# Optimization experiments

Hardware: AMD Instinct MI355X
Metric: run time of the kernel (lower is better)

The kernel has to match this reference:

```python
import jax, jax.numpy as jnp
import numpy as np
import math

B, L, D, H, FF = 32, 512, 512, 8, 2048
DH = D // H
EPS = 1e-5

def pe_table(L, D):
    pos = jnp.arange(L, dtype=jnp.float32)[:, None]
    div = jnp.exp(jnp.arange(0, D, 2, dtype=jnp.float32) * (-(math.log(10000.0) / D)))
    pe = jnp.zeros((L, D), dtype=jnp.float32)
    pe = pe.at[:, 0::2].set(jnp.sin(pos * div))
    pe = pe.at[:, 1::2].set(jnp.cos(pos * div))
    return pe

def setup_inputs() -> dict:
    key = jax.random.key(0)
    ks = jax.random.split(key, 16)
    s = 0.02
    inp = {
        "x": jax.random.normal(ks[0], (B, L, D), jnp.float32),
        "mask": jnp.ones((B, L), jnp.int32),
        "speaker_emb": jax.random.normal(ks[1], (B, L, D), jnp.float32),
        "Wg": jax.random.normal(ks[2], (D, D), jnp.float32) * s,
        "Wq": jax.random.normal(ks[3], (D, D), jnp.float32) * s,
        "bq": jnp.zeros((D,), jnp.float32),
        "Wk": jax.random.normal(ks[4], (D, D), jnp.float32) * s,
        "bk": jnp.zeros((D,), jnp.float32),
        "Wv": jax.random.normal(ks[5], (D, D), jnp.float32) * s,
        "bv": jnp.zeros((D,), jnp.float32),
        "Wo": jax.random.normal(ks[6], (D, D), jnp.float32) * s,
        "bo": jnp.zeros((D,), jnp.float32),
        "ln_g": jnp.ones((D,), jnp.float32),
        "ln_b": jnp.zeros((D,), jnp.float32),
        "W1": jax.random.normal(ks[7], (FF, D), jnp.float32) * s,
        "b1": jnp.zeros((FF,), jnp.float32),
        "W2": jax.random.normal(ks[8], (D, FF), jnp.float32) * s,
        "b2": jnp.zeros((D,), jnp.float32),
    }
    return inp

def layer_norm(x, g, b):
    mu = jnp.mean(x, axis=-1, keepdims=True)
    var = jnp.var(x, axis=-1, keepdims=True)
    return (x - mu) * jax.lax.rsqrt(var + EPS) * g + b

def reference(x, mask, speaker_emb, Wg, Wq, bq, Wk, bk, Wv, bv, Wo, bo, ln_g, ln_b, W1, b1, W2, b2):
    # DynamicGating: sigmoid(x W^T) * x
    x = jax.nn.sigmoid(x @ Wg.T) * x
    # speaker embedding + sinusoidal positional encoding (dropout is eval/no-op)
    x = x + speaker_emb + pe_table(L, D)[None, :, :]
    # Multi-head self-attention (eager, full score matrix)
    q = (x @ Wq.T + bq).reshape(B, L, H, DH).transpose(0, 2, 1, 3) / math.sqrt(DH)
    k = (x @ Wk.T + bk).reshape(B, L, H, DH).transpose(0, 2, 1, 3)
    v = (x @ Wv.T + bv).reshape(B, L, H, DH).transpose(0, 2, 1, 3)
    scores = jnp.einsum("bhqd,bhkd->bhqk", q, k)  # (B,H,L,L)
    key_mask = (mask == 0)[:, None, None, :]  # mask keys where mask==0
    scores = jnp.where(key_mask, jnp.float32(-1e10), scores)
    attn = jax.nn.softmax(scores, axis=-1)
    ctx = jnp.einsum("bhqk,bhkd->bhqd", attn, v)
    ctx = ctx.transpose(0, 2, 1, 3).reshape(B, L, D)
    attn_out = ctx @ Wo.T + bo
    h = attn_out + x  # residual (dropout no-op)
    # FeedForwardNet: note GELU applied after BOTH linears (faithful to source)
    mid = jax.nn.gelu(layer_norm(h, ln_g, ln_b) @ W1.T + b1, approximate=True)
    out = jax.nn.gelu(mid @ W2.T + b2, approximate=True)
    return out + h
```

## Files before the change

### kernel.cpp

```cpp
#include <hip/hip_runtime.h>
#include <math.h>

#define Bn 32
#define Ln 512
#define Dn 512
#define Hn 8
#define DHn 64
#define FFn 2048
#define Mn (Bn*Ln)
#define QKVS 1536

typedef __attribute__((ext_vector_type(4))) float f32x4;
typedef __attribute__((ext_vector_type(8))) short short8;

__device__ __forceinline__ float bf2f(ushort u){ return __uint_as_float(((unsigned)u) << 16); }
__device__ __forceinline__ ushort f2bf(float f){
  unsigned u = __float_as_uint(f);
  u += 0x7FFFu + ((u >> 16) & 1u);
  return (ushort)(u >> 16);
}
__device__ __forceinline__ float gelu_fast(float x){
  float y2 = 1.5957691216057308f * (x + 0.044715f*x*x*x);
  return x / (1.0f + __expf(-y2));
}

__device__ __forceinline__ void gload_lds16(const ushort* g, ushort* l){
  __builtin_amdgcn_global_load_lds(
      (__attribute__((address_space(1))) void*)(void*)g,
      (__attribute__((address_space(3))) void*)(void*)l, 16, 0, 0);
}

__device__ __forceinline__ void cvt4(const float* __restrict__ in, ushort* __restrict__ out, int u){
  float4 v = *(const float4*)(in + u*4);
  ushort4 o;
  o.x = f2bf(v.x); o.y = f2bf(v.y); o.z = f2bf(v.z); o.w = f2bf(v.w);
  *(ushort4*)(out + u*4) = o;
}

__global__ __launch_bounds__(256) void prep_kernel(
    const float* __restrict__ Wg, const float* __restrict__ Wq, const float* __restrict__ Wk,
    const float* __restrict__ Wv, const float* __restrict__ Wo, const float* __restrict__ W1,
    const float* __restrict__ W2,
    const float* __restrict__ bq, const float* __restrict__ bk, const float* __restrict__ bv,
    ushort* __restrict__ wgb, ushort* __restrict__ wqkvb, ushort* __restrict__ wob,
    ushort* __restrict__ w1b, ushort* __restrict__ w2b,
    float* __restrict__ pe, float* __restrict__ bqkv)
{
  int u = blockIdx.x*256 + threadIdx.x;
  const int WU = 65536, FU = 262144;
  if (u < WU){ cvt4(Wg, wgb, u); return; }            u -= WU;
  if (u < WU){ cvt4(Wq, wqkvb, u); return; }          u -= WU;
  if (u < WU){ cvt4(Wk, wqkvb + 262144, u); return; } u -= WU;
  if (u < WU){ cvt4(Wv, wqkvb + 524288, u); return; } u -= WU;
  if (u < WU){ cvt4(Wo, wob, u); return; }            u -= WU;
  if (u < FU){ cvt4(W1, w1b, u); return; }            u -= FU;
  if (u < FU){ cvt4(W2, w2b, u); return; }            u -= FU;
  if (u < WU){
    int e = u*4; int l = e >> 9; int d0 = e & 511;
    #pragma unroll
    for (int p=0;p<2;p++){
      int i = (d0 >> 1) + p;
      float dv = expf((float)(2*i) * (-9.210340371976184f/512.0f));
      float ang = (float)l * dv;
      pe[e + 2*p]     = sinf(ang);
      pe[e + 2*p + 1] = cosf(ang);
    }
    return;
  }
  u -= WU;
  if (u < 384){
    int e = u*4;
    #pragma unroll
    for (int j=0;j<4;j++){
      int i = e + j;
      bqkv[i] = (i < 512) ? bq[i] : (i < 1024) ? bk[i-512] : bv[i-1024];
    }
  }
}

__global__ void cvt_kernel(const float* __restrict__ in, ushort* __restrict__ out, int n){
  int i = (blockIdx.x*256 + threadIdx.x)*4;
  if (i >= n) return;
  cvt4(in, out, i >> 2);
}

template<int MODE>
__global__ __launch_bounds__(512) void gemm_kernel(
    const ushort* __restrict__ A, const ushort* __restrict__ W,
    const float* __restrict__ bias,
    const float* __restrict__ res,
    const ushort* __restrict__ rbf,
    const float* __restrict__ spk, const float* __restrict__ pe,
    float* __restrict__ outf, ushort* __restrict__ outb, ushort* __restrict__ outb2,
    int K, int N, int gx)
{
  __shared__ ushort lbuf[2][2][16384];
  int t = threadIdx.x;
  int wave = t >> 6, lane = t & 63;
  int wrow = wave >> 2, wcol = wave & 3;
  int g = lane >> 4, r16 = lane & 15;

  int nwg = gx * (Mn/256);
  int wg = blockIdx.x;
  int tile = (wg & 7)*(nwg >> 3) + (wg >> 3);
  int trow = tile / gx;
  int tcol = tile - trow*gx;
  int rowBase = trow * 256;
  int colBase = tcol * 256;

  int srow8 = lane >> 3;
  int sucol = ((lane & 7) ^ srow8) * 8;
  const ushort* gA = A + (size_t)(rowBase + wave*8 + srow8)*K + sucol;
  const ushort* gW = W + (size_t)(colBase + wave*8 + srow8)*K + sucol;

  f32x4 acc[8][4];
  #pragma unroll
  for (int m=0;m<8;m++)
    #pragma unroll
    for (int n=0;n<4;n++) acc[m][n] = (f32x4)0.0f;

  #pragma unroll
  for (int c=0;c<4;c++){
    gload_lds16(gA + (size_t)c*64*K, &lbuf[0][0][c*4096 + wave*512]);
    gload_lds16(gW + (size_t)c*64*K, &lbuf[0][1][c*4096 + wave*512]);
  }

  int cb = 0;
  for (int k0 = 0; k0 < K; k0 += 64){
    if (k0 + 64 < K){
      #pragma unroll
      for (int c=0;c<4;c++){
        gload_lds16(gA + (size_t)c*64*K + k0 + 64, &lbuf[cb^1][0][c*4096 + wave*512]);
        gload_lds16(gW + (size_t)c*64*K + k0 + 64, &lbuf[cb^1][1][c*4096 + wave*512]);
      }
      asm volatile("s_waitcnt vmcnt(8)" ::: "memory");
    } else {
      asm volatile("s_waitcnt vmcnt(0)" ::: "memory");
    }
    __builtin_amdgcn_s_barrier();
    #pragma unroll
    for (int ks=0; ks<2; ks++){
      short8 af[8], bfr[4];
      #pragma unroll
      for (int m=0;m<8;m++){
        int row = wrow*128 + m*16 + r16;
        af[m] = *(const short8*)&lbuf[cb][0][row*64 + (((ks<<2)+g) ^ (r16 & 7))*8];
      }
      #pragma unroll
      for (int n=0;n<4;n++){
        int row = wcol*64 + n*16 + r16;
        bfr[n] = *(const short8*)&lbuf[cb][1][row*64 + (((ks<<2)+g) ^ (r16 & 7))*8];
      }
      #pragma unroll
      for (int m=0;m<8;m++)
        #pragma unroll
        for (int n=0;n<4;n++)
          acc[m][n] = __builtin_amdgcn_mfma_f32_16x16x32_bf16(af[m], bfr[n], acc[m][n], 0, 0, 0);
    }
    __builtin_amdgcn_s_barrier();
    cb ^= 1;
  }

  if constexpr (MODE == 0 || MODE == 1 || MODE == 3){
    bool vpart = false;
    if constexpr (MODE == 1) vpart = (colBase >= 1024);
    if (!vpart){
      ushort* ct = &lbuf[0][0][0];
      #pragma unroll
      for (int m=0;m<8;m++){
        #pragma unroll
        for (int n=0;n<4;n++){
          int col = wcol*64 + n*16 + r16;
          int gc = colBase + col;
          float sc = 1.0f;
          if constexpr (MODE == 1) sc = (gc < 512) ? 0.125f : 1.0f;
          #pragma unroll
          for (int j=0;j<4;j++){
            int row = wrow*128 + m*16 + g*4 + j;
            float c = acc[m][n][j];
            ushort val;
            if constexpr (MODE == 0){
              int gr = rowBase + row;
              size_t o = (size_t)gr * N + gc;
              float s = 1.0f/(1.0f + __expf(-c));
              val = f2bf(s * res[o] + spk[o] + pe[(gr & (Ln-1))*Dn + gc]);
            } else if constexpr (MODE == 3){
              val = f2bf(gelu_fast(c + bias[gc]));
            } else {
              val = f2bf((c + bias[gc]) * sc);
            }
            ct[row*256 + (col ^ ((row & 7) << 3))] = val;
          }
        }
      }
      __syncthreads();
      int r = t >> 1, ch = (t & 1)*128;
      ushort* dst = outb + (size_t)(rowBase + r)*N + colBase + ch;
      #pragma unroll
      for (int q=0;q<16;q++){
        int col = (ch + q*8) ^ ((r & 7) << 3);
        *(short8*)(dst + q*8) = *(const short8*)&ct[r*256 + col];
      }
    } else {
      #pragma unroll
      for (int m=0;m<8;m++){
        #pragma unroll
        for (int n=0;n<4;n++){
          int gc = colBase + wcol*64 + n*16 + r16;
          int dhg = gc - 1024;
          int gr0 = rowBase + wrow*128 + m*16 + g*4;
          int bb = gr0 >> 9, l0 = gr0 & 511;
          ushort4 o4;
          o4.x = f2bf(acc[m][n][0] + bias[gc]);
          o4.y = f2bf(acc[m][n][1] + bias[gc]);
          o4.z = f2bf(acc[m][n][2] + bias[gc]);
          o4.w = f2bf(acc[m][n][3] + bias[gc]);
          *(ushort4*)(outb2 + ((size_t)(bb*Hn + (dhg>>6))*DHn + (dhg & 63))*Ln + l0) = o4;
        }
      }
    }
  } else {
    #pragma unroll
    for (int m=0;m<8;m++){
      #pragma unroll
      for (int n=0;n<4;n++){
        int gc = colBase + wcol*64 + n*16 + r16;
        #pragma unroll
        for (int j=0;j<4;j++){
          int gr = rowBase + wrow*128 + m*16 + g*4 + j;
          size_t o = (size_t)gr * N + gc;
          float c = acc[m][n][j];
          if constexpr (MODE == 2){
            outf[o] = c + bias[gc] + bf2f(rbf[o]);
          } else {
            outf[o] = gelu_fast(c + bias[gc]) + res[o];
          }
        }
      }
    }
  }
}

__global__ __launch_bounds__(256) void attn_mfma_kernel(
    const ushort* __restrict__ qb, const ushort* __restrict__ kb, const ushort* __restrict__ vtb,
    const int* __restrict__ mask, ushort* __restrict__ ctxb)
{
  __shared__ ushort lK[2][64][72];
  __shared__ ushort lVt[2][64][72];
  __shared__ ushort lP[4][32][72];

  int t = threadIdx.x;
  int w = t >> 6, lane = t & 63;
  int g = lane >> 4, r16 = lane & 15;
  int b = blockIdx.z, h = blockIdx.y;
  int qbase = blockIdx.x*128 + w*32;

  int key0 = t >> 3;
  int c8s = (t & 7) * 8;
  const ushort* kbase = kb + (size_t)(b*Ln)*QKVS + h*DHn + c8s;
  const ushort* vt = vtb + (size_t)((b*Hn + h)*DHn) * Ln;

  short8 af_q[2][2];
  #pragma unroll
  for (int m=0;m<2;m++)
    #pragma unroll
    for (int ks=0;ks<2;ks++)
      af_q[m][ks] = *(const short8*)(qb + (size_t)(b*Ln + qbase + m*16 + r16)*QKVS + h*DHn + ks*32 + g*8);

  f32x4 acc_ctx[2][4];
  #pragma unroll
  for (int m=0;m<2;m++)
    #pragma unroll
    for (int n=0;n<4;n++) acc_ctx[m][n] = (f32x4)0.0f;
  float mrun[2][4], lrun[2][4];
  #pragma unroll
  for (int m=0;m<2;m++)
    #pragma unroll
    for (int j=0;j<4;j++){ mrun[m][j] = -INFINITY; lrun[m][j] = 0.0f; }

  {
    short8 ka = *(const short8*)(kbase + (size_t)key0*QKVS);
    short8 kc = *(const short8*)(kbase + (size_t)(key0+32)*QKVS);
    short8 va = *(const short8*)(vt + (size_t)key0*Ln + c8s);
    short8 vc = *(const short8*)(vt + (size_t)(key0+32)*Ln + c8s);
    *(short8*)&lK[0][key0][c8s] = ka;
    *(short8*)&lK[0][key0+32][c8s] = kc;
    *(short8*)&lVt[0][key0][c8s] = va;
    *(short8*)&lVt[0][key0+32][c8s] = vc;
  }
  __syncthreads();
  int cb = 0;

  for (int kb0 = 0; kb0 < Ln; kb0 += 64){
    short8 kna, knb, vna, vnb;
    bool more = (kb0 + 64 < Ln);
    if (more){
      kna = *(const short8*)(kbase + (size_t)(kb0 + 64 + key0)*QKVS);
      knb = *(const short8*)(kbase + (size_t)(kb0 + 64 + key0 + 32)*QKVS);
      vna = *(const short8*)(vt + (size_t)key0*Ln + kb0 + 64 + c8s);
      vnb = *(const short8*)(vt + (size_t)(key0+32)*Ln + kb0 + 64 + c8s);
    }

    f32x4 acc_s[2][4];
    #pragma unroll
    for (int m=0;m<2;m++)
      #pragma unroll
      for (int n=0;n<4;n++) acc_s[m][n] = (f32x4)0.0f;
    __builtin_amdgcn_s_setprio(1);
    #pragma unroll
    for (int ks=0;ks<2;ks++){
      short8 bf_k[4];
      #pragma unroll
      for (int n=0;n<4;n++)
        bf_k[n] = *(const short8*)&lK[cb][n*16 + r16][ks*32 + g*8];
      #pragma unroll
      for (int m=0;m<2;m++)
        #pragma unroll
        for (int n=0;n<4;n++)
          acc_s[m][n] = __builtin_amdgcn_mfma_f32_16x16x32_bf16(af_q[m][ks], bf_k[n], acc_s[m][n], 0, 0, 0);
    }
    __builtin_amdgcn_s_setprio(0);

    #pragma unroll
    for (int n=0;n<4;n++){
      if (mask[b*Ln + kb0 + n*16 + r16] == 0){
        #pragma unroll
        for (int m=0;m<2;m++)
          #pragma unroll
          for (int j=0;j<4;j++) acc_s[m][n][j] = -1e10f;
      }
    }

    #pragma unroll
    for (int m=0;m<2;m++){
      #pragma unroll
      for (int j=0;j<4;j++){
        float tmax = fmaxf(fmaxf(acc_s[m][0][j], acc_s[m][1][j]),
                           fmaxf(acc_s[m][2][j], acc_s[m][3][j]));
        #pragma unroll
        for (int off=1; off<16; off<<=1) tmax = fmaxf(tmax, __shfl_xor(tmax, off));
        float newm = fmaxf(mrun[m][j], tmax);
        float alpha = __expf(mrun[m][j] - newm);
        float p0 = __expf(acc_s[m][0][j] - newm);
        float p1 = __expf(acc_s[m][1][j] - newm);
        float p2 = __expf(acc_s[m][2][j] - newm);
        float p3 = __expf(acc_s[m][3][j] - newm);
        float tsum = (p0+p1)+(p2+p3);
        #pragma unroll
        for (int off=1; off<16; off<<=1) tsum += __shfl_xor(tsum, off);
        lrun[m][j] = lrun[m][j]*alpha + tsum;
        mrun[m][j] = newm;
        #pragma unroll
        for (int n2=0;n2<4;n2++) acc_ctx[m][n2][j] *= alpha;
        int prow = m*16 + g*4 + j;
        lP[w][prow][0*16 + r16] = f2bf(p0);
        lP[w][prow][1*16 + r16] = f2bf(p1);
        lP[w][prow][2*16 + r16] = f2bf(p2);
        lP[w][prow][3*16 + r16] = f2bf(p3);
      }
    }

    __builtin_amdgcn_s_setprio(1);
    #pragma unroll
    for (int ks2=0;ks2<2;ks2++){
      short8 af_p[2], bf_v[4];
      #pragma unroll
      for (int m=0;m<2;m++)
        af_p[m] = *(const short8*)&lP[w][m*16 + r16][ks2*32 + g*8];
      #pragma unroll
      for (int n=0;n<4;n++)
        bf_v[n] = *(const short8*)&lVt[cb][n*16 + r16][ks2*32 + g*8];
      #pragma unroll
      for (int m=0;m<2;m++)
        #pragma unroll
        for (int n=0;n<4;n++)
          acc_ctx[m][n] = __builtin_amdgcn_mfma_f32_16x16x32_bf16(af_p[m], bf_v[n], acc_ctx[m][n], 0, 0, 0);
    }
    __builtin_amdgcn_s_setprio(0);

    if (more){
      *(short8*)&lK[cb^1][key0][c8s] = kna;
      *(short8*)&lK[cb^1][key0+32][c8s] = knb;
      *(short8*)&lVt[cb^1][key0][c8s] = vna;
      *(short8*)&lVt[cb^1][key0+32][c8s] = vnb;
    }
    __syncthreads();
    cb ^= 1;
  }

  #pragma unroll
  for (int m=0;m<2;m++){
    #pragma unroll
    for (int j=0;j<4;j++){
      float inv = 1.0f / lrun[m][j];
      int gr = qbase + m*16 + g*4 + j;
      #pragma unroll
      for (int n=0;n<4;n++){
        ctxb[(size_t)(b*Ln + gr)*Dn + h*DHn + n*16 + r16] = f2bf(acc_ctx[m][n][j] * inv);
      }
    }
  }
}

__global__ __launch_bounds__(256) void ln_kernel(
    const float* __restrict__ hbuf, const float* __restrict__ gamma, const float* __restrict__ beta,
    ushort* __restrict__ out)
{
  int row = blockIdx.x*4 + (threadIdx.x >> 6);
  int lane = threadIdx.x & 63;
  const float* p = hbuf + (size_t)row*Dn + lane*8;
  float4 a = *(const float4*)p;
  float4 c = *(const float4*)(p + 4);
  float v[8] = {a.x,a.y,a.z,a.w,c.x,c.y,c.z,c.w};
  float s = 0.f, ss = 0.f;
  #pragma unroll
  for (int j=0;j<8;j++){ s += v[j]; ss += v[j]*v[j]; }
  #pragma unroll
  for (int off=32; off>0; off>>=1){ s += __shfl_xor(s, off); ss += __shfl_xor(ss, off); }
  float mu = s * (1.0f/Dn);
  float var = ss * (1.0f/Dn) - mu*mu;
  float rstd = rsqrtf(var + 1e-5f);
  ushort o8[8];
  #pragma unroll
  for (int j=0;j<8;j++) o8[j] = f2bf((v[j]-mu)*rstd*gamma[lane*8+j] + beta[lane*8+j]);
  ushort* op = out + (size_t)row*Dn + lane*8;
  *(ushort4*)op       = make_ushort4(o8[0],o8[1],o8[2],o8[3]);
  *(ushort4*)(op + 4) = make_ushort4(o8[4],o8[5],o8[6],o8[7]);
}

extern "C" void kernel_launch(void* const* d_in, const int* in_sizes, int n_in,
                              void* d_out, int out_size, void* d_ws, size_t ws_size,
                              hipStream_t stream) {
  (void)in_sizes; (void)n_in; (void)out_size; (void)ws_size;
  const float* x    = (const float*)d_in[0];
  const int*   mask = (const int*)d_in[1];
  const float* spk  = (const float*)d_in[2];
  const float* Wg   = (const float*)d_in[3];
  const float* Wq   = (const float*)d_in[4];  const float* bq = (const float*)d_in[5];
  const float* Wk   = (const float*)d_in[6];  const float* bk = (const float*)d_in[7];
  const float* Wv   = (const float*)d_in[8];  const float* bv = (const float*)d_in[9];
  const float* Wo   = (const float*)d_in[10]; const float* bo = (const float*)d_in[11];
  const float* lng  = (const float*)d_in[12]; const float* lnbeta = (const float*)d_in[13];
  const float* W1   = (const float*)d_in[14]; const float* b1 = (const float*)d_in[15];
  const float* W2   = (const float*)d_in[16]; const float* b2 = (const float*)d_in[17];
  float* out = (float*)d_out;

  char* w = (char*)d_ws;
  size_t o = 0;
  ushort* xbf   = (ushort*)(w + o); o += (size_t)Mn*Dn*2;
  ushort* xinb  = (ushort*)(w + o); o += (size_t)Mn*Dn*2;
  ushort* qkvb  = (ushort*)(w + o); o += (size_t)Mn*QKVS*2;
  ushort* vtb   = (ushort*)(w + o); o += (size_t)Mn*Dn*2;
  ushort* ctxb  = (ushort*)(w + o); o += (size_t)Mn*Dn*2;
  float*  hbuf  = (float*)(w + o);  o += (size_t)Mn*Dn*4;
  ushort* lnbuf = (ushort*)(w + o); o += (size_t)Mn*Dn*2;
  ushort* wgb   = (ushort*)(w + o); o += (size_t)Dn*Dn*2;
  ushort* wqkvb = (ushort*)(w + o); o += (size_t)QKVS*Dn*2;
  ushort* wob   = (ushort*)(w + o); o += (size_t)Dn*Dn*2;
  ushort* w1b   = (ushort*)(w + o); o += (size_t)FFn*Dn*2;
  ushort* w2b   = (ushort*)(w + o); o += (size_t)Dn*FFn*2;
  float*  pebuf = (float*)(w + o);  o += (size_t)Ln*Dn*4;
  float*  bqkv  = (float*)(w + o);  o += (size_t)QKVS*4;
  ushort* midb  = xbf;

  hipLaunchKernelGGL(prep_kernel, dim3(3586), dim3(256), 0, stream,
                     Wg, Wq, Wk, Wv, Wo, W1, W2, bq, bk, bv,
                     wgb, wqkvb, wob, w1b, w2b, pebuf, bqkv);
  hipLaunchKernelGGL(cvt_kernel, dim3((Mn*Dn/4)/256), dim3(256), 0, stream, x, xbf, Mn*Dn);

  hipLaunchKernelGGL((gemm_kernel<0>), dim3((Dn/256)*(Mn/256)), dim3(512), 0, stream,
                     xbf, wgb, (const float*)nullptr, x, (const ushort*)nullptr, spk, pebuf,
                     (float*)nullptr, xinb, (ushort*)nullptr, Dn, Dn, Dn/256);
  hipLaunchKernelGGL((gemm_kernel<1>), dim3((QKVS/256)*(Mn/256)), dim3(512), 0, stream,
                     xinb, wqkvb, bqkv, (const float*)nullptr, (const ushort*)nullptr,
                     (const float*)nullptr, (const float*)nullptr,
                     (float*)nullptr, qkvb, vtb, Dn, QKVS, QKVS/256);
  hipLaunchKernelGGL(attn_mfma_kernel, dim3(Ln/128, Hn, Bn), dim3(256), 0, stream,
                     qkvb, qkvb + 512, vtb, mask, ctxb);
  hipLaunchKernelGGL((gemm_kernel<2>), dim3((Dn/256)*(Mn/256)), dim3(512), 0, stream,
                     ctxb, wob, bo, (const float*)nullptr, xinb, (const float*)nullptr,
                     (const float*)nullptr, hbuf, (ushort*)nullptr, (ushort*)nullptr, Dn, Dn, Dn/256);
  hipLaunchKernelGGL(ln_kernel, dim3(Mn/4), dim3(256), 0, stream, hbuf, lng, lnbeta, lnbuf);
  hipLaunchKernelGGL((gemm_kernel<3>), dim3((FFn/256)*(Mn/256)), dim3(512), 0, stream,
                     lnbuf, w1b, b1, (const float*)nullptr, (const ushort*)nullptr,
                     (const float*)nullptr, (const float*)nullptr,
                     (float*)nullptr, midb, (ushort*)nullptr, Dn, FFn, FFn/256);
  hipLaunchKernelGGL((gemm_kernel<4>), dim3((Dn/256)*(Mn/256)), dim3(512), 0, stream,
                     midb, w2b, b2, hbuf, (const ushort*)nullptr,
                     (const float*)nullptr, (const float*)nullptr,
                     out, (ushort*)nullptr, (ushort*)nullptr, FFn, Dn, Dn/256);
}
```

Baseline: 347.3 us.

## Use 256x128 GEMM tiles with three-stage LDS pipeline and MFMA priority

Narrows the GEMM output tile from 256x256 to 256x128, doubling the workgroup count. It replaces the double-buffered LDS loop with a three-stage ring so loads for tile k+2 are in flight while tile k is computed, and drops one barrier per iteration. It also raises wave priority around the MFMA block. The intent is better occupancy and CU fill on the small-N GEMMs and more latency hiding, at the cost of lower arithmetic intensity per tile and more redundant A-tile loads.

```diff
diff --git a/kernel.cpp b/kernel.cpp
--- a/kernel.cpp
+++ b/kernel.cpp
@@ -94,7 +94,7 @@
     float* __restrict__ outf, ushort* __restrict__ outb, ushort* __restrict__ outb2,
     int K, int N, int gx)
 {
-  __shared__ ushort lbuf[2][2][16384];
+  __shared__ ushort lbuf[3][24576];
   int t = threadIdx.x;
   int wave = t >> 6, lane = t & 63;
   int wrow = wave >> 2, wcol = wave & 3;
@@ -106,71 +106,84 @@
   int trow = tile / gx;
   int tcol = tile - trow*gx;
   int rowBase = trow * 256;
-  int colBase = tcol * 256;
+  int colBase = tcol * 128;
 
   int srow8 = lane >> 3;
   int sucol = ((lane & 7) ^ srow8) * 8;
   const ushort* gA = A + (size_t)(rowBase + wave*8 + srow8)*K + sucol;
   const ushort* gW = W + (size_t)(colBase + wave*8 + srow8)*K + sucol;
 
-  f32x4 acc[8][4];
+  int NT = K >> 6;
+
+  f32x4 acc[8][2];
   #pragma unroll
   for (int m=0;m<8;m++)
     #pragma unroll
-    for (int n=0;n<4;n++) acc[m][n] = (f32x4)0.0f;
-
-  #pragma unroll
-  for (int c=0;c<4;c++){
-    gload_lds16(gA + (size_t)c*64*K, &lbuf[0][0][c*4096 + wave*512]);
-    gload_lds16(gW + (size_t)c*64*K, &lbuf[0][1][c*4096 + wave*512]);
-  }
-
-  int cb = 0;
-  for (int k0 = 0; k0 < K; k0 += 64){
-    if (k0 + 64 < K){
-      #pragma unroll
-      for (int c=0;c<4;c++){
-        gload_lds16(gA + (size_t)c*64*K + k0 + 64, &lbuf[cb^1][0][c*4096 + wave*512]);
-        gload_lds16(gW + (size_t)c*64*K + k0 + 64, &lbuf[cb^1][1][c*4096 + wave*512]);
-      }
-      asm volatile("s_waitcnt vmcnt(8)" ::: "memory");
-    } else {
-      asm volatile("s_waitcnt vmcnt(0)" ::: "memory");
-    }
-    __builtin_amdgcn_s_barrier();
+    for (int n=0;n<2;n++) acc[m][n] = (f32x4)0.0f;
+
+  #pragma unroll
+  for (int c=0;c<4;c++) gload_lds16(gA + (size_t)c*64*K,      &lbuf[0][c*4096 + wave*512]);
+  #pragma unroll
+  for (int c=0;c<2;c++) gload_lds16(gW + (size_t)c*64*K,      &lbuf[0][16384 + c*4096 + wave*512]);
+  #pragma unroll
+  for (int c=0;c<4;c++) gload_lds16(gA + (size_t)c*64*K + 64, &lbuf[1][c*4096 + wave*512]);
+  #pragma unroll
+  for (int c=0;c<2;c++) gload_lds16(gW + (size_t)c*64*K + 64, &lbuf[1][16384 + c*4096 + wave*512]);
+  asm volatile("s_waitcnt vmcnt(6)" ::: "memory");
+  __builtin_amdgcn_s_barrier();
+
+  int cur = 0, stg = 2;
+  for (int kt = 0; kt < NT; ++kt){
+    if (kt + 2 < NT){
+      int k0 = (kt + 2) << 6;
+      #pragma unroll
+      for (int c=0;c<4;c++) gload_lds16(gA + (size_t)c*64*K + k0, &lbuf[stg][c*4096 + wave*512]);
+      #pragma unroll
+      for (int c=0;c<2;c++) gload_lds16(gW + (size_t)c*64*K + k0, &lbuf[stg][16384 + c*4096 + wave*512]);
+    }
+    const ushort* ab = &lbuf[cur][0];
+    const ushort* bb = &lbuf[cur][16384];
+    __builtin_amdgcn_s_setprio(1);
     #pragma unroll
     for (int ks=0; ks<2; ks++){
-      short8 af[8], bfr[4];
+      short8 af[8], bfr[2];
       #pragma unroll
       for (int m=0;m<8;m++){
         int row = wrow*128 + m*16 + r16;
-        af[m] = *(const short8*)&lbuf[cb][0][row*64 + (((ks<<2)+g) ^ (r16 & 7))*8];
-      }
-      #pragma unroll
-      for (int n=0;n<4;n++){
-        int row = wcol*64 + n*16 + r16;
-        bfr[n] = *(const short8*)&lbuf[cb][1][row*64 + (((ks<<2)+g) ^ (r16 & 7))*8];
+        af[m] = *(const short8*)&ab[row*64 + (((ks<<2)+g) ^ (row & 7))*8];
+      }
+      #pragma unroll
+      for (int n=0;n<2;n++){
+        int row = wcol*32 + n*16 + r16;
+        bfr[n] = *(const short8*)&bb[row*64 + (((ks<<2)+g) ^ (row & 7))*8];
       }
       #pragma unroll
       for (int m=0;m<8;m++)
         #pragma unroll
-        for (int n=0;n<4;n++)
+        for (int n=0;n<2;n++)
           acc[m][n] = __builtin_amdgcn_mfma_f32_16x16x32_bf16(af[m], bfr[n], acc[m][n], 0, 0, 0);
     }
-    __builtin_amdgcn_s_barrier();
-    cb ^= 1;
+    __builtin_amdgcn_s_setprio(0);
+    if (kt + 1 < NT){
+      if (kt + 2 < NT) asm volatile("s_waitcnt vmcnt(6)" ::: "memory");
+      else             asm volatile("s_waitcnt vmcnt(0)" ::: "memory");
+      __builtin_amdgcn_s_barrier();
+    }
+    cur = (cur == 2) ? 0 : cur + 1;
+    stg = (stg == 2) ? 0 : stg + 1;
   }
 
   if constexpr (MODE == 0 || MODE == 1 || MODE == 3){
     bool vpart = false;
     if constexpr (MODE == 1) vpart = (colBase >= 1024);
     if (!vpart){
-      ushort* ct = &lbuf[0][0][0];
+      __syncthreads();
+      ushort* ct = &lbuf[0][0];
       #pragma unroll
       for (int m=0;m<8;m++){
         #pragma unroll
-        for (int n=0;n<4;n++){
-          int col = wcol*64 + n*16 + r16;
+        for (int n=0;n<2;n++){
+          int col = wcol*32 + n*16 + r16;
           int gc = colBase + col;
           float sc = 1.0f;
           if constexpr (MODE == 1) sc = (gc < 512) ? 0.125f : 1.0f;
@@ -189,33 +202,33 @@
             } else {
               val = f2bf((c + bias[gc]) * sc);
             }
-            ct[row*256 + (col ^ ((row & 7) << 3))] = val;
+            ct[row*128 + (col ^ ((row & 7) << 3))] = val;
           }
         }
       }
       __syncthreads();
-      int r = t >> 1, ch = (t & 1)*128;
+      int r = t >> 1, ch = (t & 1)*64;
       ushort* dst = outb + (size_t)(rowBase + r)*N + colBase + ch;
       #pragma unroll
-      for (int q=0;q<16;q++){
+      for (int q=0;q<8;q++){
         int col = (ch + q*8) ^ ((r & 7) << 3);
-        *(short8*)(dst + q*8) = *(const short8*)&ct[r*256 + col];
+        *(short8*)(dst + q*8) = *(const short8*)&ct[r*128 + col];
       }
     } else {
       #pragma unroll
       for (int m=0;m<8;m++){
         #pragma unroll
-        for (int n=0;n<4;n++){
-          int gc = colBase + wcol*64 + n*16 + r16;
+        for (int n=0;n<2;n++){
+          int gc = colBase + wcol*32 + n*16 + r16;
           int dhg = gc - 1024;
           int gr0 = rowBase + wrow*128 + m*16 + g*4;
-          int bb = gr0 >> 9, l0 = gr0 & 511;
+          int bb2 = gr0 >> 9, l0 = gr0 & 511;
           ushort4 o4;
           o4.x = f2bf(acc[m][n][0] + bias[gc]);
           o4.y = f2bf(acc[m][n][1] + bias[gc]);
           o4.z = f2bf(acc[m][n][2] + bias[gc]);
           o4.w = f2bf(acc[m][n][3] + bias[gc]);
-          *(ushort4*)(outb2 + ((size_t)(bb*Hn + (dhg>>6))*DHn + (dhg & 63))*Ln + l0) = o4;
+          *(ushort4*)(outb2 + ((size_t)(bb2*Hn + (dhg>>6))*DHn + (dhg & 63))*Ln + l0) = o4;
         }
       }
     }
@@ -223,8 +236,8 @@
     #pragma unroll
     for (int m=0;m<8;m++){
       #pragma unroll
-      for (int n=0;n<4;n++){
-        int gc = colBase + wcol*64 + n*16 + r16;
+      for (int n=0;n<2;n++){
+        int gc = colBase + wcol*32 + n*16 + r16;
         #pragma unroll
         for (int j=0;j<4;j++){
           int gr = rowBase + wrow*128 + m*16 + g*4 + j;
@@ -468,25 +481,25 @@
                      wgb, wqkvb, wob, w1b, w2b, pebuf, bqkv);
   hipLaunchKernelGGL(cvt_kernel, dim3((Mn*Dn/4)/256), dim3(256), 0, stream, x, xbf, Mn*Dn);
 
-  hipLaunchKernelGGL((gemm_kernel<0>), dim3((Dn/256)*(Mn/256)), dim3(512), 0, stream,
+  hipLaunchKernelGGL((gemm_kernel<0>), dim3((Dn/128)*(Mn/256)), dim3(512), 0, stream,
                      xbf, wgb, (const float*)nullptr, x, (const ushort*)nullptr, spk, pebuf,
-                     (float*)nullptr, xinb, (ushort*)nullptr, Dn, Dn, Dn/256);
-  hipLaunchKernelGGL((gemm_kernel<1>), dim3((QKVS/256)*(Mn/256)), dim3(512), 0, stream,
+                     (float*)nullptr, xinb, (ushort*)nullptr, Dn, Dn, Dn/128);
+  hipLaunchKernelGGL((gemm_kernel<1>), dim3((QKVS/128)*(Mn/256)), dim3(512), 0, stream,
                      xinb, wqkvb, bqkv, (const float*)nullptr, (const ushort*)nullptr,
                      (const float*)nullptr, (const float*)nullptr,
-                     (float*)nullptr, qkvb, vtb, Dn, QKVS, QKVS/256);
+                     (float*)nullptr, qkvb, vtb, Dn, QKVS, QKVS/128);
   hipLaunchKernelGGL(attn_mfma_kernel, dim3(Ln/128, Hn, Bn), dim3(256), 0, stream,
                      qkvb, qkvb + 512, vtb, mask, ctxb);
-  hipLaunchKernelGGL((gemm_kernel<2>), dim3((Dn/256)*(Mn/256)), dim3(512), 0, stream,
+  hipLaunchKernelGGL((gemm_kernel<2>), dim3((Dn/128)*(Mn/256)), dim3(512), 0, stream,
                      ctxb, wob, bo, (const float*)nullptr, xinb, (const float*)nullptr,
-                     (const float*)nullptr, hbuf, (ushort*)nullptr, (ushort*)nullptr, Dn, Dn, Dn/256);
+                     (const float*)nullptr, hbuf, (ushort*)nullptr, (ushort*)nullptr, Dn, Dn, Dn/128);
   hipLaunchKernelGGL(ln_kernel, dim3(Mn/4), dim3(256), 0, stream, hbuf, lng, lnbeta, lnbuf);
-  hipLaunchKernelGGL((gemm_kernel<3>), dim3((FFn/256)*(Mn/256)), dim3(512), 0, stream,
+  hipLaunchKernelGGL((gemm_kernel<3>), dim3((FFn/128)*(Mn/256)), dim3(512), 0, stream,
                      lnbuf, w1b, b1, (const float*)nullptr, (const ushort*)nullptr,
                      (const float*)nullptr, (const float*)nullptr,
-                     (float*)nullptr, midb, (ushort*)nullptr, Dn, FFn, FFn/256);
-  hipLaunchKernelGGL((gemm_kernel<4>), dim3((Dn/256)*(Mn/256)), dim3(512), 0, stream,
+                     (float*)nullptr, midb, (ushort*)nullptr, Dn, FFn, FFn/128);
+  hipLaunchKernelGGL((gemm_kernel<4>), dim3((Dn/128)*(Mn/256)), dim3(512), 0, stream,
                      midb, w2b, b2, hbuf, (const ushort*)nullptr,
                      (const float*)nullptr, (const float*)nullptr,
-                     out, (ushort*)nullptr, (ushort*)nullptr, FFn, Dn, Dn/256);
-}
+                     out, (ushort*)nullptr, (ushort*)nullptr, FFn, Dn, Dn/128);
+}
```

Result: faster. 324.0 us (-6.7%).
